# Optimization experiments

Hardware: AMD Instinct MI355X
Metric: run time of the kernel (lower is better)

Reference implementation:

```python
import jax, jax.numpy as jnp
import numpy as np

B, N, H, S, NSEC = 1, 8192, 256, 128, 8
TAU = 0.5
DEPTH_LO, DEPTH_HI = 0.0, 2.4
PADDING = 0.1
EPS = 1e-6
_p = float(np.clip(TAU, 1e-4, 1.0 - 1e-4))
LOGIT_TAU = float(np.log(_p / (1.0 - _p)))


def mlp(p, W1, b1, W2, b2, W3, b3, W4, b4):
    # p: [..., 3] -> logit [...]
    h = jax.nn.softplus(p @ W1 + b1)
    h = jax.nn.softplus(h @ W2 + b2)
    h = jax.nn.softplus(h @ W3 + b3)
    return (h @ W4 + b4)[..., 0]


def cube_intersection(ray0, rd):
    # Faithful port of check_ray_intersection_with_unit_cube.
    p_dist = 0.5 + PADDING / 2.0
    plane = jnp.concatenate([jnp.full((3,), p_dist), jnp.full((3,), -p_dist)])  # (6,)
    nom = plane - jnp.tile(ray0, (1, 1, 2))          # (B,N,6)
    den = jnp.tile(rd, (1, 1, 2))
    den = jnp.where(jnp.abs(den) < 1e-9, 1e-9, den)  # numerical guard
    d_int = nom / den                                 # (B,N,6)
    p_int = ray0[:, :, None, :] + d_int[..., None] * rd[:, :, None, :]  # (B,N,6,3)
    inside = jnp.all(jnp.abs(p_int) <= p_dist + EPS, axis=-1)           # (B,N,6)
    mask = inside.sum(-1) == 2                                           # rays hitting cube
    # pick the (exactly two) intersecting planes in ascending plane order,
    # matching torch boolean indexing semantics
    plane_id = jnp.arange(6)
    key = jnp.where(inside, plane_id, plane_id + 6)
    idx2 = jnp.argsort(key, axis=-1)[..., :2]                            # (B,N,2)
    p2 = jnp.take_along_axis(p_int, idx2[..., None], axis=2)            # (B,N,2,3)
    norm_rd = jnp.linalg.norm(rd, axis=-1)                               # (B,N)
    d2 = jnp.linalg.norm(p2 - ray0[:, :, None, :], axis=-1) / norm_rd[..., None]
    d2 = jnp.where(mask[..., None], d2, 0.0)
    d2 = jnp.sort(d2, axis=-1)
    return d2, mask


def _secant(d_low, f_low, d_high, f_high):
    den = f_high - f_low
    den = jnp.where(jnp.abs(den) < 1e-12, 1e-12, den)
    return -f_low * (d_high - d_low) / den + d_low


def reference(ray0, ray_direction, W1, b1, W2, b2, W3, b3, W4, b4):
    rd = ray_direction
    dec = lambda p: mlp(p, W1, b1, W2, b2, W3, b3, W4, b4)
    sg = jax.lax.stop_gradient

    # ---- proposal depths (no grad, as torch no_grad ray-marching) ----
    t = jnp.linspace(0.0, 1.0, S)                       # (S,)
    d_default = DEPTH_LO + t * (DEPTH_HI - DEPTH_LO)
    d2, mask_cube = cube_intersection(ray0, rd)
    d_cube = d2[..., 0:1] + t * (d2[..., 1:2] - d2[..., 0:1])   # (B,N,S)
    d_prop = jnp.where(mask_cube[..., None], d_cube, d_default)
    d_prop = sg(d_prop)

    p_prop = sg(ray0)[:, :, None, :] + d_prop[..., None] * sg(rd)[:, :, None, :]
    val = sg(dec(p_prop)) - LOGIT_TAU                   # (B,N,S)

    mask_0_not_occupied = val[..., 0] < 0
    sign_matrix = jnp.concatenate(
        [jnp.sign(val[..., :-1] * val[..., 1:]), jnp.ones(val.shape[:-1] + (1,), val.dtype)], -1)
    cost = sign_matrix * jnp.arange(S, 0, -1, dtype=val.dtype)
    idx = jnp.argmin(cost, -1)                          # first sign-change step
    vmin = jnp.min(cost, -1)
    f_low = jnp.take_along_axis(val, idx[..., None], -1)[..., 0]
    mask = (vmin < 0) & (f_low < 0) & mask_0_not_occupied

    idx_hi = jnp.minimum(idx + 1, S - 1)
    d_low = jnp.take_along_axis(d_prop, idx[..., None], -1)[..., 0]
    d_high = jnp.take_along_axis(d_prop, idx_hi[..., None], -1)[..., 0]
    f_high = jnp.take_along_axis(val, idx_hi[..., None], -1)[..., 0]

    # ---- secant refinement (no grad in torch) ----
    r0s, rds = sg(ray0), sg(rd)
    d_pred = _secant(d_low, f_low, d_high, f_high)
    for _ in range(NSEC):
        f_mid = sg(dec(r0s + d_pred[..., None] * rds)) - LOGIT_TAU
        low = f_mid < 0
        d_low = jnp.where(low, d_pred, d_low)
        f_low = jnp.where(low, f_mid, f_low)
        d_high = jnp.where(low, d_high, d_pred)
        f_high = jnp.where(low, f_high, f_mid)
        d_pred = _secant(d_low, f_low, d_high, f_high)

    # ---- differentiable implicit-gradient correction (analytic backward of
    # DepthFunction: dd/dtheta = -(df/dtheta)/(df/dd) at the surface point) ----
    d_star = sg(d_pred)
    f_of_d = lambda d: dec(ray0 + d[..., None] * rd) - LOGIT_TAU
    f_val = f_of_d(d_star)                              # differentiable wrt params/rays
    _, df_dd = jax.jvp(f_of_d, (d_star,), (jnp.ones_like(d_star),))
    df_dd = sg(df_dd)
    df_dd = jnp.where(jnp.abs(df_dd) < 1e-6,
                      jnp.where(df_dd < 0, -1e-6, 1e-6), df_dd)
    d_out = d_star - f_val / df_dd
    d_final = jnp.where(mask, d_out, 0.0)
    return d_final


def setup_inputs() -> dict:
    key = jax.random.key(0)
    ks = jax.random.split(key, 10)
    origin = jnp.array([0.0, 0.0, -1.5])
    ray0 = origin + 0.01 * jax.random.normal(ks[0], (B, N, 3), dtype=jnp.float32)
    target = jax.random.uniform(ks[1], (B, N, 3), minval=-0.4, maxval=0.4, dtype=jnp.float32)
    rd = target - ray0
    rd = rd / jnp.linalg.norm(rd, axis=-1, keepdims=True)
    W1 = jax.random.normal(ks[2], (3, H), dtype=jnp.float32) / jnp.sqrt(3.0)
    b1 = 0.1 * jax.random.normal(ks[3], (H,), dtype=jnp.float32)
    W2 = jax.random.normal(ks[4], (H, H), dtype=jnp.float32) / jnp.sqrt(float(H))
    b2 = 0.1 * jax.random.normal(ks[5], (H,), dtype=jnp.float32)
    W3 = jax.random.normal(ks[6], (H, H), dtype=jnp.float32) / jnp.sqrt(float(H))
    b3 = 0.1 * jax.random.normal(ks[7], (H,), dtype=jnp.float32)
    W4 = jax.random.normal(ks[8], (H, 1), dtype=jnp.float32) / jnp.sqrt(float(H))
    b4 = 0.1 * jax.random.normal(ks[9], (1,), dtype=jnp.float32)
    return {"ray0": ray0, "ray_direction": rd, "W1": W1, "b1": b1,
            "W2": W2, "b2": b2, "W3": W3, "b3": b3, "W4": W4, "b4": b4}
```

## Files before the change

### kernel.cpp

```cpp
#include <hip/hip_runtime.h>
#include <math.h>

#define NRAY 8192
#define SSAMP 128
#define HD 256
#define AROW 264
#define A1ROW 40
#define FIXCAP 262144
#define FIXTHR 0.018f

typedef short s16x8 __attribute__((ext_vector_type(8)));
typedef float f32x4 __attribute__((ext_vector_type(4)));

__device__ __forceinline__ unsigned short f2bf(float f) {
    unsigned u = __float_as_uint(f);
    u += 0x7fffu + ((u >> 16) & 1u);
    return (unsigned short)(u >> 16);
}
__device__ __forceinline__ float bf2f(unsigned short s) {
    return __uint_as_float(((unsigned)s) << 16);
}
__device__ __forceinline__ void split2(float f, unsigned short& hi, unsigned short& lo) {
    unsigned u = __float_as_uint(f);
    hi = (unsigned short)(u >> 16);
    float r = f - __uint_as_float(u & 0xFFFF0000u);
    lo = f2bf(r);
}
__device__ __forceinline__ unsigned pack_bf16x2(float a, float b) {
    unsigned r;
    asm("v_cvt_pk_bf16_f32 %0, %1, %2" : "=v"(r) : "v"(a), "v"(b));
    return r;
}
__device__ __forceinline__ float softplus_fast(float x) {
    return fmaxf(x, 0.0f) + __logf(1.0f + __expf(-fabsf(x)));
}
__device__ __forceinline__ float softplus_cheap(float x) {
    float m = __expf(-fabsf(x));
    float p = fmaf(m, fmaf(0.14258f, m, -0.44943f), 1.0f);
    return fmaxf(x, 0.0f) + m * p;
}
__device__ __forceinline__ float sigmoid_fast(float x) {
    return 1.0f / (1.0f + __expf(-x));
}

__global__ __launch_bounds__(256)
void prep_kernel(const float* __restrict__ W1, const float* __restrict__ b1,
                 const float* __restrict__ W2, const float* __restrict__ W3,
                 const float* __restrict__ ray0, const float* __restrict__ rdg,
                 unsigned short* __restrict__ P2, unsigned short* __restrict__ P3,
                 unsigned short* __restrict__ B1, float* __restrict__ rayinfo,
                 int* __restrict__ fix_cnt) {
    const int b = blockIdx.x, tid = threadIdx.x;
    if (b < 256) {
        int idx = b * 256 + tid;
        int k = idx >> 8, n = idx & 255;
        int nt = n >> 4, kt = k >> 5, lq = (k >> 3) & 3, j = k & 7;
        int lane = (lq << 4) | (n & 15);
        size_t off = (size_t)((nt * 8 + kt) * 2) * 512 + (size_t)lane * 8 + j;
        float w = W2[idx];
        unsigned short hi = f2bf(w);
        P2[off] = hi; P2[off + 512] = f2bf(w - bf2f(hi));
        w = W3[idx];
        hi = f2bf(w);
        P3[off] = hi; P3[off + 512] = f2bf(w - bf2f(hi));
    } else if (b < 288) {
        int idx = (b - 256) * 256 + tid;
        int w = idx & 511;
        int lane = w >> 3, j = w & 7;
        int k = ((lane >> 4) << 3) + j;
        int n = ((idx >> 9) << 4) + (lane & 15);
        unsigned short s = 0;
        if (k < 3) s = f2bf(W1[k * HD + n]);
        else if (k == 3) s = f2bf(b1[n]);
        else if (k < 7) s = f2bf(W1[(k - 4) * HD + n]);
        else if (k == 7) { unsigned short bh = f2bf(b1[n]); s = f2bf(b1[n] - bf2f(bh)); }
        else if (k < 11) { float wv = W1[(k - 8) * HD + n]; unsigned short wh = f2bf(wv); s = f2bf(wv - bf2f(wh)); }
        B1[idx] = s;
    } else {
        int r = (b - 288) * 256 + tid;
        if (r == 0) *fix_cnt = 0;
        float o0 = ray0[3 * r], o1 = ray0[3 * r + 1], o2 = ray0[3 * r + 2];
        float v0 = rdg[3 * r], v1 = rdg[3 * r + 1], v2 = rdg[3 * r + 2];
        const float pd = 0.55f, lim = pd + 1e-6f;
        float di[6]; int insk[6]; int cnt = 0;
        for (int k = 0; k < 6; k++) {
            int a = k % 3;
            float pl = (k < 3) ? pd : -pd;
            float den = (a == 0) ? v0 : ((a == 1) ? v1 : v2);
            if (fabsf(den) < 1e-9f) den = 1e-9f;
            float oa = (a == 0) ? o0 : ((a == 1) ? o1 : o2);
            float dd = (pl - oa) / den;
            float px = o0 + dd * v0, py = o1 + dd * v1, pz = o2 + dd * v2;
            int ins = (fabsf(px) <= lim) && (fabsf(py) <= lim) && (fabsf(pz) <= lim);
            di[k] = dd; insk[k] = ins; cnt += ins;
        }
        float d0 = 0.f, sl = 2.4f;
        if (cnt == 2) {
            int k1 = -1, k2 = -1;
            for (int k = 0; k < 6; k++) if (insk[k]) { if (k1 < 0) k1 = k; else k2 = k; }
            float nrd = sqrtf(v0 * v0 + v1 * v1 + v2 * v2);
            float ax = di[k1] * v0, ay = di[k1] * v1, az = di[k1] * v2;
            float d1n = sqrtf(ax * ax + ay * ay + az * az) / nrd;
            float bx = di[k2] * v0, by = di[k2] * v1, bz = di[k2] * v2;
            float d2n = sqrtf(bx * bx + by * by + bz * bz) / nrd;
            d0 = fminf(d1n, d2n);
            sl = fmaxf(d1n, d2n) - d0;
        }
        float* ri = rayinfo + (size_t)r * 8;
        ri[0] = d0; ri[1] = sl;
        ri[2] = o0; ri[3] = o1; ri[4] = o2;
        ri[5] = v0; ri[6] = v1; ri[7] = v2;
    }
}


template<int MT>
__device__ __forceinline__ void gemm_l1(const unsigned short* A1,
                                        const unsigned short* __restrict__ B1,
                                        f32x4 acc[MT][4], int lane, int ntbase) {
    const int r15 = lane & 15, q = lane >> 4;
    s16x8 wh[4];
#pragma unroll
    for (int nt = 0; nt < 4; nt++)
        wh[nt] = *(((const s16x8*)B1) + (size_t)(ntbase + nt) * 64 + lane);
#pragma unroll
    for (int mt = 0; mt < MT; mt++) {
        s16x8 ah = *(const s16x8*)(A1 + (mt * 16 + r15) * A1ROW + q * 8);
#pragma unroll
        for (int nt = 0; nt < 4; nt++)
            acc[mt][nt] = __builtin_amdgcn_mfma_f32_16x16x32_bf16(wh[nt], ah, (f32x4){0.f,0.f,0.f,0.f}, 0, 0, 0);
    }
}

template<int MT>
__device__ __forceinline__ void gemm_1t(const unsigned short* Act,
                                        const unsigned short* __restrict__ Wp,
                                        f32x4 acc[MT][4], int lane, int ntbase) {
#pragma unroll
    for (int mt = 0; mt < MT; mt++)
#pragma unroll
        for (int nt = 0; nt < 4; nt++) acc[mt][nt] = (f32x4){0.f, 0.f, 0.f, 0.f};
    const int r15 = lane & 15, q = lane >> 4;
#pragma unroll 2
    for (int kt = 0; kt < 8; kt++) {
        s16x8 wh[4];
#pragma unroll
        for (int nt = 0; nt < 4; nt++) {
            const s16x8* wp = ((const s16x8*)Wp) + (size_t)((ntbase + nt) * 8 + kt) * 128 + lane;
            wh[nt] = wp[0];
        }
        const int kc = kt * 32 + q * 8;
#pragma unroll
        for (int mt = 0; mt < MT; mt++) {
            s16x8 ah = *(const s16x8*)(Act + (mt * 16 + r15) * AROW + kc);
#pragma unroll
            for (int nt = 0; nt < 4; nt++)
                acc[mt][nt] = __builtin_amdgcn_mfma_f32_16x16x32_bf16(wh[nt], ah, acc[mt][nt], 0, 0, 0);
        }
    }
}

template<int MT>
__device__ __forceinline__ void gemm_3t(const unsigned short* Ahi, const unsigned short* Alo,
                                        const unsigned short* __restrict__ Wp,
                                        f32x4 acc[MT][4], int lane, int ntbase) {
#pragma unroll
    for (int mt = 0; mt < MT; mt++)
#pragma unroll
        for (int nt = 0; nt < 4; nt++) acc[mt][nt] = (f32x4){0.f, 0.f, 0.f, 0.f};
    const int r15 = lane & 15, q = lane >> 4;
#pragma unroll 2
    for (int kt = 0; kt < 8; kt++) {
        s16x8 wh[4], wl[4];
#pragma unroll
        for (int nt = 0; nt < 4; nt++) {
            const s16x8* wp = ((const s16x8*)Wp) + (size_t)((ntbase + nt) * 8 + kt) * 128 + lane;
            wh[nt] = wp[0];
            wl[nt] = wp[64];
        }
        const int kc = kt * 32 + q * 8;
#pragma unroll
        for (int mt = 0; mt < MT; mt++) {
            s16x8 ah = *(const s16x8*)(Ahi + (mt * 16 + r15) * AROW + kc);
            s16x8 al = *(const s16x8*)(Alo + (mt * 16 + r15) * AROW + kc);
#pragma unroll
            for (int nt = 0; nt < 4; nt++) {
                acc[mt][nt] = __builtin_amdgcn_mfma_f32_16x16x32_bf16(wh[nt], ah, acc[mt][nt], 0, 0, 0);
                acc[mt][nt] = __builtin_amdgcn_mfma_f32_16x16x32_bf16(wl[nt], ah, acc[mt][nt], 0, 0, 0);
                acc[mt][nt] = __builtin_amdgcn_mfma_f32_16x16x32_bf16(wh[nt], al, acc[mt][nt], 0, 0, 0);
            }
        }
    }
}

template<int MT>
__device__ __forceinline__ void gemm_dual(const unsigned short* Avh, const unsigned short* Avl,
                                          const unsigned short* Ath, const unsigned short* Atl,
                                          const unsigned short* __restrict__ Wp,
                                          f32x4 av[MT][4], f32x4 at[MT][4], int lane, int ntbase) {
#pragma unroll
    for (int mt = 0; mt < MT; mt++)
#pragma unroll
        for (int nt = 0; nt < 4; nt++) {
            av[mt][nt] = (f32x4){0.f, 0.f, 0.f, 0.f};
            at[mt][nt] = (f32x4){0.f, 0.f, 0.f, 0.f};
        }
    const int r15 = lane & 15, q = lane >> 4;
#pragma unroll 2
    for (int kt = 0; kt < 8; kt++) {
        s16x8 wh[4], wl[4];
#pragma unroll
        for (int nt = 0; nt < 4; nt++) {
            const s16x8* wp = ((const s16x8*)Wp) + (size_t)((ntbase + nt) * 8 + kt) * 128 + lane;
            wh[nt] = wp[0];
            wl[nt] = wp[64];
        }
        const int kc = kt * 32 + q * 8;
#pragma unroll
        for (int mt = 0; mt < MT; mt++) {
            s16x8 avhf = *(const s16x8*)(Avh + (mt * 16 + r15) * AROW + kc);
            s16x8 avlf = *(const s16x8*)(Avl + (mt * 16 + r15) * AROW + kc);
            s16x8 athf = *(const s16x8*)(Ath + (mt * 16 + r15) * AROW + kc);
            s16x8 atlf = *(const s16x8*)(Atl + (mt * 16 + r15) * AROW + kc);
#pragma unroll
            for (int nt = 0; nt < 4; nt++) {
                av[mt][nt] = __builtin_amdgcn_mfma_f32_16x16x32_bf16(wh[nt], avhf, av[mt][nt], 0, 0, 0);
                av[mt][nt] = __builtin_amdgcn_mfma_f32_16x16x32_bf16(wl[nt], avhf, av[mt][nt], 0, 0, 0);
                av[mt][nt] = __builtin_amdgcn_mfma_f32_16x16x32_bf16(wh[nt], avlf, av[mt][nt], 0, 0, 0);
                at[mt][nt] = __builtin_amdgcn_mfma_f32_16x16x32_bf16(wh[nt], athf, at[mt][nt], 0, 0, 0);
                at[mt][nt] = __builtin_amdgcn_mfma_f32_16x16x32_bf16(wl[nt], athf, at[mt][nt], 0, 0, 0);
                at[mt][nt] = __builtin_amdgcn_mfma_f32_16x16x32_bf16(wh[nt], atlf, at[mt][nt], 0, 0, 0);
            }
        }
    }
}

template<int MT>
__device__ __forceinline__ void epi_l1(f32x4 acc[MT][4], unsigned short* Ahi, int lane, int wn0) {
    const int r15 = lane & 15, q = lane >> 4;
#pragma unroll
    for (int mt = 0; mt < MT; mt++) {
        unsigned short* rowp = Ahi + (mt * 16 + r15) * AROW + wn0 + q * 4;
#pragma unroll
        for (int nt = 0; nt < 4; nt++) {
            float h0 = softplus_cheap(acc[mt][nt][0]);
            float h1 = softplus_cheap(acc[mt][nt][1]);
            float h2 = softplus_cheap(acc[mt][nt][2]);
            float h3 = softplus_cheap(acc[mt][nt][3]);
            *reinterpret_cast<uint2*>(rowp + nt * 16) =
                make_uint2(pack_bf16x2(h0, h1), pack_bf16x2(h2, h3));
        }
    }
}

template<int MT>
__device__ __forceinline__ void epi_l1_sp(f32x4 acc[MT][4], unsigned short* Ahi, unsigned short* Alo,
                                          int lane, int wn0) {
    const int r15 = lane & 15, q = lane >> 4;
#pragma unroll
    for (int mt = 0; mt < MT; mt++) {
        const int rowoff = (mt * 16 + r15) * AROW + wn0 + q * 4;
#pragma unroll
        for (int nt = 0; nt < 4; nt++) {
            float h0 = softplus_fast(acc[mt][nt][0]);
            float h1 = softplus_fast(acc[mt][nt][1]);
            float h2 = softplus_fast(acc[mt][nt][2]);
            float h3 = softplus_fast(acc[mt][nt][3]);
            unsigned x0 = pack_bf16x2(h0, h1), x1 = pack_bf16x2(h2, h3);
            float l0 = h0 - __uint_as_float(x0 << 16);
            float l1 = h1 - __uint_as_float(x0 & 0xFFFF0000u);
            float l2 = h2 - __uint_as_float(x1 << 16);
            float l3 = h3 - __uint_as_float(x1 & 0xFFFF0000u);
            *reinterpret_cast<uint2*>(Ahi + rowoff + nt * 16) = make_uint2(x0, x1);
            *reinterpret_cast<uint2*>(Alo + rowoff + nt * 16) =
                make_uint2(pack_bf16x2(l0, l1), pack_bf16x2(l2, l3));
        }
    }
}

template<int MT>
__device__ __forceinline__ void epi_hidden_1t(f32x4 acc[MT][4], const float* __restrict__ b,
                                              unsigned short* Ahi, int lane, int wn0) {
    const int r15 = lane & 15, q = lane >> 4;
    f32x4 bb[4];
#pragma unroll
    for (int nt = 0; nt < 4; nt++) bb[nt] = *(const f32x4*)(b + wn0 + nt * 16 + q * 4);
#pragma unroll
    for (int mt = 0; mt < MT; mt++) {
        unsigned short* rowp = Ahi + (mt * 16 + r15) * AROW + wn0 + q * 4;
#pragma unroll
        for (int nt = 0; nt < 4; nt++) {
            float h0 = softplus_cheap(acc[mt][nt][0] + bb[nt][0]);
            float h1 = softplus_cheap(acc[mt][nt][1] + bb[nt][1]);
            float h2 = softplus_cheap(acc[mt][nt][2] + bb[nt][2]);
            float h3 = softplus_cheap(acc[mt][nt][3] + bb[nt][3]);
            *reinterpret_cast<uint2*>(rowp + nt * 16) =
                make_uint2(pack_bf16x2(h0, h1), pack_bf16x2(h2, h3));
        }
    }
}

template<int MT>
__device__ __forceinline__ void epi_hidden_sp(f32x4 acc[MT][4], const float* __restrict__ b,
                                              unsigned short* Ahi, unsigned short* Alo,
                                              int lane, int wn0) {
    const int r15 = lane & 15, q = lane >> 4;
    f32x4 bb[4];
#pragma unroll
    for (int nt = 0; nt < 4; nt++) bb[nt] = *(const f32x4*)(b + wn0 + nt * 16 + q * 4);
#pragma unroll
    for (int mt = 0; mt < MT; mt++) {
        const int rowoff = (mt * 16 + r15) * AROW + wn0 + q * 4;
#pragma unroll
        for (int nt = 0; nt < 4; nt++) {
            float h0 = softplus_fast(acc[mt][nt][0] + bb[nt][0]);
            float h1 = softplus_fast(acc[mt][nt][1] + bb[nt][1]);
            float h2 = softplus_fast(acc[mt][nt][2] + bb[nt][2]);
            float h3 = softplus_fast(acc[mt][nt][3] + bb[nt][3]);
            unsigned x0 = pack_bf16x2(h0, h1), x1 = pack_bf16x2(h2, h3);
            float l0 = h0 - __uint_as_float(x0 << 16);
            float l1 = h1 - __uint_as_float(x0 & 0xFFFF0000u);
            float l2 = h2 - __uint_as_float(x1 << 16);
            float l3 = h3 - __uint_as_float(x1 & 0xFFFF0000u);
            *reinterpret_cast<uint2*>(Ahi + rowoff + nt * 16) = make_uint2(x0, x1);
            *reinterpret_cast<uint2*>(Alo + rowoff + nt * 16) =
                make_uint2(pack_bf16x2(l0, l1), pack_bf16x2(l2, l3));
        }
    }
}

template<int MT>
__device__ __forceinline__ void epi_dual(f32x4 av[MT][4], f32x4 at[MT][4], const float* __restrict__ b,
                                         unsigned short* Avh, unsigned short* Avl,
                                         unsigned short* Ath, unsigned short* Atl,
                                         int lane, int wn0) {
    const int r15 = lane & 15, q = lane >> 4;
    f32x4 bb[4];
#pragma unroll
    for (int nt = 0; nt < 4; nt++) bb[nt] = *(const f32x4*)(b + wn0 + nt * 16 + q * 4);
#pragma unroll
    for (int mt = 0; mt < MT; mt++) {
        const int rowoff = (mt * 16 + r15) * AROW + wn0 + q * 4;
#pragma unroll
        for (int nt = 0; nt < 4; nt++) {
            float h[4], g[4];
#pragma unroll
            for (int r = 0; r < 4; r++) {
                float z = av[mt][nt][r] + bb[nt][r];
                h[r] = softplus_fast(z);
                g[r] = sigmoid_fast(z) * at[mt][nt][r];
            }
            unsigned x0 = pack_bf16x2(h[0], h[1]), x1 = pack_bf16x2(h[2], h[3]);
            float l0 = h[0] - __uint_as_float(x0 << 16);
            float l1 = h[1] - __uint_as_float(x0 & 0xFFFF0000u);
            float l2 = h[2] - __uint_as_float(x1 << 16);
            float l3 = h[3] - __uint_as_float(x1 & 0xFFFF0000u);
            *reinterpret_cast<uint2*>(Avh + rowoff + nt * 16) = make_uint2(x0, x1);
            *reinterpret_cast<uint2*>(Avl + rowoff + nt * 16) =
                make_uint2(pack_bf16x2(l0, l1), pack_bf16x2(l2, l3));
            x0 = pack_bf16x2(g[0], g[1]); x1 = pack_bf16x2(g[2], g[3]);
            l0 = g[0] - __uint_as_float(x0 << 16);
            l1 = g[1] - __uint_as_float(x0 & 0xFFFF0000u);
            l2 = g[2] - __uint_as_float(x1 << 16);
            l3 = g[3] - __uint_as_float(x1 & 0xFFFF0000u);
            *reinterpret_cast<uint2*>(Ath + rowoff + nt * 16) = make_uint2(x0, x1);
            *reinterpret_cast<uint2*>(Atl + rowoff + nt * 16) =
                make_uint2(pack_bf16x2(l0, l1), pack_bf16x2(l2, l3));
        }
    }
}

template<int MT, bool CH>
__device__ __forceinline__ void l4_reduce(f32x4 acc[MT][4], const float* __restrict__ b3,
                                          const float* __restrict__ W4,
                                          float* partial, int lane, int wn0) {
    const int r15 = lane & 15, q = lane >> 4;
    f32x4 w4v[4], b3v[4];
#pragma unroll
    for (int nt = 0; nt < 4; nt++) {
        w4v[nt] = *(const f32x4*)(W4 + wn0 + nt * 16 + q * 4);
        b3v[nt] = *(const f32x4*)(b3 + wn0 + nt * 16 + q * 4);
    }
#pragma unroll
    for (int mt = 0; mt < MT; mt++) {
        float p = 0.f;
#pragma unroll
        for (int nt = 0; nt < 4; nt++)
#pragma unroll
            for (int r = 0; r < 4; r++) {
                float z = acc[mt][nt][r] + b3v[nt][r];
                float h = CH ? softplus_cheap(z) : softplus_fast(z);
                p = fmaf(h, w4v[nt][r], p);
            }
        p += __shfl_xor(p, 16, 64);
        p += __shfl_xor(p, 32, 64);
        if (q == 0) partial[mt * 16 + r15] = p;
    }
}

template<int MT>
__device__ __forceinline__ void l4_reduce_dual(f32x4 av[MT][4], f32x4 at[MT][4],
                                               const float* __restrict__ b3, const float* __restrict__ W4,
                                               float* pv, float* pt, int lane, int wn0) {
    const int r15 = lane & 15, q = lane >> 4;
    f32x4 w4v[4], b3v[4];
#pragma unroll
    for (int nt = 0; nt < 4; nt++) {
        w4v[nt] = *(const f32x4*)(W4 + wn0 + nt * 16 + q * 4);
        b3v[nt] = *(const f32x4*)(b3 + wn0 + nt * 16 + q * 4);
    }
#pragma unroll
    for (int mt = 0; mt < MT; mt++) {
        float sv = 0.f, st = 0.f;
#pragma unroll
        for (int nt = 0; nt < 4; nt++)
#pragma unroll
            for (int r = 0; r < 4; r++) {
                float z = av[mt][nt][r] + b3v[nt][r];
                sv = fmaf(softplus_fast(z), w4v[nt][r], sv);
                st = fmaf(sigmoid_fast(z) * at[mt][nt][r], w4v[nt][r], st);
            }
        sv += __shfl_xor(sv, 16, 64);
        sv += __shfl_xor(sv, 32, 64);
        st += __shfl_xor(st, 16, 64);
        st += __shfl_xor(st, 32, 64);
        if (q == 0) {
            pv[mt * 16 + r15] = sv;
            pt[mt * 16 + r15] = st;
        }
    }
}

__global__ __launch_bounds__(256, 4)
void coarse_mfma(const float* __restrict__ rayinfo,
                 const unsigned short* __restrict__ B1,
                 const unsigned short* __restrict__ P2, const float* __restrict__ b2,
                 const unsigned short* __restrict__ P3, const float* __restrict__ b3,
                 const float* __restrict__ W4, const float* __restrict__ b4,
                 float* __restrict__ val_out, float* __restrict__ dprop_out,
                 int* __restrict__ fix_cnt, int* __restrict__ fix_list) {
    __shared__ __align__(16) unsigned short Ahi[64 * AROW];
    __shared__ __align__(16) unsigned short A1[64 * A1ROW];
    float* partial = (float*)A1;
    const int tid = threadIdx.x;
    const int lane = tid & 63, wave = tid >> 6;
    const int r = blockIdx.x >> 1, half = blockIdx.x & 1;

    if (tid < 64) {
        const float* ri = rayinfo + (size_t)r * 8;
        const int s = half * 64 + tid;
        float t = (float)s * (1.0f / 127.0f);
        float d = fmaf(t, ri[1], ri[0]);
        dprop_out[r * SSAMP + s] = d;
        float px = fmaf(d, ri[5], ri[2]);
        float py = fmaf(d, ri[6], ri[3]);
        float pz = fmaf(d, ri[7], ri[4]);
        unsigned short hx, lx, hy, ly, hz, lz;
        split2(px, hx, lx); split2(py, hy, ly); split2(pz, hz, lz);
        unsigned short* row = A1 + tid * A1ROW;
        row[0] = hx; row[1] = hy; row[2] = hz; row[3] = 0x3F80u;
        row[4] = lx; row[5] = ly; row[6] = lz; row[7] = 0x3F80u;
        row[8] = hx; row[9] = hy; row[10] = hz;
#pragma unroll
        for (int c = 11; c < 32; c++) row[c] = 0;
    }
    __syncthreads();
    f32x4 acc[4][4];
    gemm_l1<4>(A1, B1, acc, lane, wave * 4);
    epi_l1<4>(acc, Ahi, lane, wave * 64);
    __syncthreads();
    gemm_1t<4>(Ahi, P2, acc, lane, wave * 4);
    __syncthreads();
    epi_hidden_1t<4>(acc, b2, Ahi, lane, wave * 64);
    __syncthreads();
    gemm_1t<4>(Ahi, P3, acc, lane, wave * 4);
    l4_reduce<4, true>(acc, b3, W4, &partial[wave * 64], lane, wave * 64);
    __syncthreads();
    if (tid < 64) {
        float v = partial[tid] + partial[64 + tid] + partial[128 + tid] + partial[192 + tid] + b4[0];
        int idx = r * SSAMP + half * 64 + tid;
        val_out[idx] = v;
        if (fabsf(v) < FIXTHR) {
            int pos = atomicAdd(fix_cnt, 1);
            if (pos < FIXCAP) fix_list[pos] = idx;
        }
    }
}

__global__ __launch_bounds__(256, 4)
void fixup3_mfma(const int* __restrict__ counter, const int* __restrict__ list,
                 float* __restrict__ val, const float* __restrict__ dprop,
                 const float* __restrict__ ray0, const float* __restrict__ rdg,
                 const unsigned short* __restrict__ B1,
                 const unsigned short* __restrict__ P2, const float* __restrict__ b2,
                 const unsigned short* __restrict__ P3, const float* __restrict__ b3,
                 const float* __restrict__ W4, const float* __restrict__ b4) {
    __shared__ __align__(16) unsigned short Ahi[32 * AROW];
    __shared__ __align__(16) unsigned short Alo[32 * AROW];
    __shared__ __align__(16) unsigned short A1[32 * A1ROW];
    __shared__ float partial[4][32];
    __shared__ int bidxs[32];
    const int cnt = min(*counter, FIXCAP);
    const int base = blockIdx.x * 32;
    if (base >= cnt) return;
    const int tid = threadIdx.x;
    const int lane = tid & 63, wave = tid >> 6;
    if (tid < 32) {
        const int i = min(base + tid, cnt - 1);
        const int bidx = list[i];
        bidxs[tid] = bidx;
        const int rr = bidx >> 7;
        float d = dprop[bidx];
        float px = ray0[3 * rr] + d * rdg[3 * rr];
        float py = ray0[3 * rr + 1] + d * rdg[3 * rr + 1];
        float pz = ray0[3 * rr + 2] + d * rdg[3 * rr + 2];
        unsigned short hx, lx, hy, ly, hz, lz;
        split2(px, hx, lx); split2(py, hy, ly); split2(pz, hz, lz);
        unsigned short* row = A1 + tid * A1ROW;
        row[0] = hx; row[1] = hy; row[2] = hz; row[3] = 0x3F80u;
        row[4] = lx; row[5] = ly; row[6] = lz; row[7] = 0x3F80u;
        row[8] = hx; row[9] = hy; row[10] = hz;
#pragma unroll
        for (int c = 11; c < 32; c++) row[c] = 0;
    }
    __syncthreads();
    f32x4 acc[2][4];
    gemm_l1<2>(A1, B1, acc, lane, wave * 4);
    epi_l1_sp<2>(acc, Ahi, Alo, lane, wave * 64);
    __syncthreads();
    gemm_3t<2>(Ahi, Alo, P2, acc, lane, wave * 4);
    __syncthreads();
    epi_hidden_sp<2>(acc, b2, Ahi, Alo, lane, wave * 64);
    __syncthreads();
    gemm_3t<2>(Ahi, Alo, P3, acc, lane, wave * 4);
    l4_reduce<2, false>(acc, b3, W4, &partial[wave][0], lane, wave * 64);
    __syncthreads();
    if (tid < 32) {
        float v = partial[0][tid] + partial[1][tid] + partial[2][tid] + partial[3][tid] + b4[0];
        val[bidxs[tid]] = v;
    }
}

__global__ __launch_bounds__(256, 4)
void refine_mfma(const float* __restrict__ val, const float* __restrict__ dprop,
                 const float* __restrict__ ray0, const float* __restrict__ rdg,
                 const float* __restrict__ W1, const float* __restrict__ b1,
                 const unsigned short* __restrict__ P2, const float* __restrict__ b2,
                 const unsigned short* __restrict__ P3, const float* __restrict__ b3,
                 const float* __restrict__ W4, const float* __restrict__ b4,
                 float* __restrict__ out) {
    __shared__ __align__(16) unsigned short Avh[16 * AROW];
    __shared__ __align__(16) unsigned short Avl[16 * AROW];
    __shared__ __align__(16) unsigned short Ath[16 * AROW];
    __shared__ __align__(16) unsigned short Atl[16 * AROW];
    __shared__ float partial[4][16], ptan[4][16];
    __shared__ float dl[16], fl[16], dh[16], fh[16], dps[16];
    __shared__ int mks[16];
    unsigned short* Ahi = Avh;
    const int tid = threadIdx.x;
    const int lane = tid & 63, wave = tid >> 6;
    const int r0 = blockIdx.x * 16;

    for (int i = 0; i < 4; i++) {
        const int r = r0 + wave * 4 + i;
        const float2 v = *(const float2*)(val + (size_t)r * SSAMP + lane * 2);
        const float2 dd = *(const float2*)(dprop + (size_t)r * SSAMP + lane * 2);
        float vnext = __shfl_down(v.x, 1, 64);
        const int s0 = lane * 2, s1 = s0 + 1;
        float pr0 = v.x * v.y;
        int sg0 = (pr0 > 0.f) ? 1 : ((pr0 < 0.f) ? -1 : 0);
        int k0 = (sg0 * (SSAMP - s0) + 129) * 256 + s0;
        int k1;
        if (lane == 63) {
            k1 = (1 + 129) * 256 + 127;
        } else {
            float pr1 = v.y * vnext;
            int sg1 = (pr1 > 0.f) ? 1 : ((pr1 < 0.f) ? -1 : 0);
            k1 = (sg1 * (SSAMP - s1) + 129) * 256 + s1;
        }
        int k = min(k0, k1);
#pragma unroll
        for (int m = 1; m < 64; m <<= 1) k = min(k, __shfl_xor(k, m, 64));
        int bidx = k & 255;
        int cmin = (k >> 8) - 129;
        int idxh = min(bidx + 1, SSAMP - 1);
        int ow = bidx >> 1, oh = idxh >> 1;
        float fa = __shfl(v.x, ow, 64), fb = __shfl(v.y, ow, 64);
        float da = __shfl(dd.x, ow, 64), db = __shfl(dd.y, ow, 64);
        float fa2 = __shfl(v.x, oh, 64), fb2 = __shfl(v.y, oh, 64);
        float da2 = __shfl(dd.x, oh, 64), db2 = __shfl(dd.y, oh, 64);
        float v0 = __shfl(v.x, 0, 64);
        if (lane == 0) {
            float f_low = (bidx & 1) ? fb : fa;
            float d_low = (bidx & 1) ? db : da;
            float f_high = (idxh & 1) ? fb2 : fa2;
            float d_high = (idxh & 1) ? db2 : da2;
            int sl = wave * 4 + i;
            mks[sl] = (cmin < 0) && (f_low < 0.f) && (v0 < 0.f);
            float den = f_high - f_low;
            if (fabsf(den) < 1e-12f) den = 1e-12f;
            dl[sl] = d_low; fl[sl] = f_low; dh[sl] = d_high; fh[sl] = f_high;
            dps[sl] = -f_low * (d_high - d_low) / den + d_low;
        }
    }
    __syncthreads();
    for (int it = 0; it < 8; it++) {
        {
            const int pt = tid >> 4, jb = (tid & 15) << 4;
            const int rr = r0 + pt;
            float d = dps[pt];
            float px = ray0[3 * rr] + d * rdg[3 * rr];
            float py = ray0[3 * rr + 1] + d * rdg[3 * rr + 1];
            float pz = ray0[3 * rr + 2] + d * rdg[3 * rr + 2];
            for (int j = jb; j < jb + 16; j += 4) {
                float4 wa = *(const float4*)(W1 + j);
                float4 wb = *(const float4*)(W1 + 256 + j);
                float4 wc = *(const float4*)(W1 + 512 + j);
                float4 bb = *(const float4*)(b1 + j);
                float z[4];
                z[0] = fmaf(px, wa.x, fmaf(py, wb.x, fmaf(pz, wc.x, bb.x)));
                z[1] = fmaf(px, wa.y, fmaf(py, wb.y, fmaf(pz, wc.y, bb.y)));
                z[2] = fmaf(px, wa.z, fmaf(py, wb.z, fmaf(pz, wc.z, bb.z)));
                z[3] = fmaf(px, wa.w, fmaf(py, wb.w, fmaf(pz, wc.w, bb.w)));
                *reinterpret_cast<uint2*>(&Ahi[pt * AROW + j]) =
                    make_uint2(pack_bf16x2(softplus_cheap(z[0]), softplus_cheap(z[1])),
                               pack_bf16x2(softplus_cheap(z[2]), softplus_cheap(z[3])));
            }
        }
        __syncthreads();
        f32x4 acc[1][4];
        gemm_1t<1>(Ahi, P2, acc, lane, wave * 4);
        __syncthreads();
        epi_hidden_1t<1>(acc, b2, Ahi, lane, wave * 64);
        __syncthreads();
        gemm_1t<1>(Ahi, P3, acc, lane, wave * 4);
        l4_reduce<1, true>(acc, b3, W4, &partial[wave][0], lane, wave * 64);
        __syncthreads();
        if (tid < 16) {
            float fm = partial[0][tid] + partial[1][tid] + partial[2][tid] + partial[3][tid] + b4[0];
            float dpv = dps[tid];
            float dlv = dl[tid], flv = fl[tid], dhv = dh[tid], fhv = fh[tid];
            if (fm < 0.f) { dlv = dpv; flv = fm; } else { dhv = dpv; fhv = fm; }
            float den = fhv - flv;
            if (fabsf(den) < 1e-12f) den = 1e-12f;
            dps[tid] = -flv * (dhv - dlv) / den + dlv;
            dl[tid] = dlv; fl[tid] = flv; dh[tid] = dhv; fh[tid] = fhv;
        }
        __syncthreads();
    }
    {
        const int pt = tid >> 4, jb = (tid & 15) << 4;
        const int rr = r0 + pt;
        float d = dps[pt];
        float v0 = rdg[3 * rr], v1 = rdg[3 * rr + 1], v2 = rdg[3 * rr + 2];
        float px = ray0[3 * rr] + d * v0;
        float py = ray0[3 * rr + 1] + d * v1;
        float pz = ray0[3 * rr + 2] + d * v2;
        for (int j = jb; j < jb + 16; j += 4) {
            float4 wa = *(const float4*)(W1 + j);
            float4 wb = *(const float4*)(W1 + 256 + j);
            float4 wc = *(const float4*)(W1 + 512 + j);
            float4 bb = *(const float4*)(b1 + j);
            float z[4], zt[4], h[4], g[4];
            z[0] = fmaf(px, wa.x, fmaf(py, wb.x, fmaf(pz, wc.x, bb.x)));
            z[1] = fmaf(px, wa.y, fmaf(py, wb.y, fmaf(pz, wc.y, bb.y)));
            z[2] = fmaf(px, wa.z, fmaf(py, wb.z, fmaf(pz, wc.z, bb.z)));
            z[3] = fmaf(px, wa.w, fmaf(py, wb.w, fmaf(pz, wc.w, bb.w)));
            zt[0] = fmaf(v0, wa.x, fmaf(v1, wb.x, v2 * wc.x));
            zt[1] = fmaf(v0, wa.y, fmaf(v1, wb.y, v2 * wc.y));
            zt[2] = fmaf(v0, wa.z, fmaf(v1, wb.z, v2 * wc.z));
            zt[3] = fmaf(v0, wa.w, fmaf(v1, wb.w, v2 * wc.w));
#pragma unroll
            for (int i = 0; i < 4; i++) {
                h[i] = softplus_fast(z[i]);
                g[i] = sigmoid_fast(z[i]) * zt[i];
            }
            unsigned x0 = pack_bf16x2(h[0], h[1]), x1 = pack_bf16x2(h[2], h[3]);
            float l0 = h[0] - __uint_as_float(x0 << 16);
            float l1 = h[1] - __uint_as_float(x0 & 0xFFFF0000u);
            float l2 = h[2] - __uint_as_float(x1 << 16);
            float l3 = h[3] - __uint_as_float(x1 & 0xFFFF0000u);
            *reinterpret_cast<uint2*>(&Avh[pt * AROW + j]) = make_uint2(x0, x1);
            *reinterpret_cast<uint2*>(&Avl[pt * AROW + j]) =
                make_uint2(pack_bf16x2(l0, l1), pack_bf16x2(l2, l3));
            x0 = pack_bf16x2(g[0], g[1]); x1 = pack_bf16x2(g[2], g[3]);
            l0 = g[0] - __uint_as_float(x0 << 16);
            l1 = g[1] - __uint_as_float(x0 & 0xFFFF0000u);
            l2 = g[2] - __uint_as_float(x1 << 16);
            l3 = g[3] - __uint_as_float(x1 & 0xFFFF0000u);
            *reinterpret_cast<uint2*>(&Ath[pt * AROW + j]) = make_uint2(x0, x1);
            *reinterpret_cast<uint2*>(&Atl[pt * AROW + j]) =
                make_uint2(pack_bf16x2(l0, l1), pack_bf16x2(l2, l3));
        }
    }
    __syncthreads();
    f32x4 av[1][4], at[1][4];
    gemm_dual<1>(Avh, Avl, Ath, Atl, P2, av, at, lane, wave * 4);
    __syncthreads();
    epi_dual<1>(av, at, b2, Avh, Avl, Ath, Atl, lane, wave * 64);
    __syncthreads();
    gemm_dual<1>(Avh, Avl, Ath, Atl, P3, av, at, lane, wave * 4);
    l4_reduce_dual<1>(av, at, b3, W4, &partial[wave][0], &ptan[wave][0], lane, wave * 64);
    __syncthreads();
    if (tid < 16) {
        float f = partial[0][tid] + partial[1][tid] + partial[2][tid] + partial[3][tid] + b4[0];
        float ft = ptan[0][tid] + ptan[1][tid] + ptan[2][tid] + ptan[3][tid];
        if (fabsf(ft) < 1e-6f) ft = (ft < 0.f) ? -1e-6f : 1e-6f;
        float dres = dps[tid] - f / ft;
        out[r0 + tid] = mks[tid] ? dres : 0.0f;
    }
}

extern "C" void kernel_launch(void* const* d_in, const int* in_sizes, int n_in,
                              void* d_out, int out_size, void* d_ws, size_t ws_size,
                              hipStream_t stream) {
    const float* ray0 = (const float*)d_in[0];
    const float* rdg  = (const float*)d_in[1];
    const float* W1 = (const float*)d_in[2];
    const float* b1 = (const float*)d_in[3];
    const float* W2 = (const float*)d_in[4];
    const float* b2 = (const float*)d_in[5];
    const float* W3 = (const float*)d_in[6];
    const float* b3 = (const float*)d_in[7];
    const float* W4 = (const float*)d_in[8];
    const float* b4 = (const float*)d_in[9];
    float* out = (float*)d_out;

    float* ws = (float*)d_ws;
    float* val    = ws;
    float* dprop  = ws + (size_t)SSAMP * NRAY;
    unsigned short* P2 = (unsigned short*)(ws + (size_t)2 * SSAMP * NRAY);
    unsigned short* P3 = P2 + 131072;
    unsigned short* B1 = P3 + 131072;
    float* rayinfo = (float*)(B1 + 8192);
    int* fix_cnt  = (int*)(rayinfo + (size_t)NRAY * 8);
    int* fix_list = fix_cnt + 64;

    hipLaunchKernelGGL(prep_kernel, dim3(320), dim3(256), 0, stream,
                       W1, b1, W2, W3, ray0, rdg, P2, P3, B1, rayinfo, fix_cnt);
    hipLaunchKernelGGL(coarse_mfma, dim3(NRAY * 2), dim3(256), 0, stream,
                       rayinfo, B1, P2, b2, P3, b3, W4, b4, val, dprop, fix_cnt, fix_list);
    hipLaunchKernelGGL(fixup3_mfma, dim3(FIXCAP / 32), dim3(256), 0, stream,
                       fix_cnt, fix_list, val, dprop, ray0, rdg,
                       B1, P2, b2, P3, b3, W4, b4);
    hipLaunchKernelGGL(refine_mfma, dim3(NRAY / 16), dim3(256), 0, stream,
                       val, dprop, ray0, rdg, W1, b1, P2, b2, P3, b3, W4, b4, out);
}
```

Before: 708.5 us.

## Split coarse MLP work across eight waves with narrower per-wave column tiles

Templates the MFMA GEMM and epilogue helpers on the number of N-tiles per wave. The coarse kernel moves to 512 threads (8 waves), with each wave covering 32 output columns instead of 64, and the final partial-sum reduction loops over 8 waves. This cuts per-wave accumulator registers and adds waves per block, aiming for more latency hiding. In exchange, weight-fragment reuse per activation load drops and the larger block means more barrier cost; the launch bound now requests 6 blocks of 512 threads per CU. The other kernels keep NT=4, so their behaviour is unchanged.

```diff
diff --git a/kernel.cpp b/kernel.cpp
--- a/kernel.cpp
+++ b/kernel.cpp
@@ -114,38 +114,38 @@
 }
 
 
-template<int MT>
+template<int MT, int NT>
 __device__ __forceinline__ void gemm_l1(const unsigned short* A1,
                                         const unsigned short* __restrict__ B1,
-                                        f32x4 acc[MT][4], int lane, int ntbase) {
-    const int r15 = lane & 15, q = lane >> 4;
-    s16x8 wh[4];
-#pragma unroll
-    for (int nt = 0; nt < 4; nt++)
+                                        f32x4 acc[MT][NT], int lane, int ntbase) {
+    const int r15 = lane & 15, q = lane >> 4;
+    s16x8 wh[NT];
+#pragma unroll
+    for (int nt = 0; nt < NT; nt++)
         wh[nt] = *(((const s16x8*)B1) + (size_t)(ntbase + nt) * 64 + lane);
 #pragma unroll
     for (int mt = 0; mt < MT; mt++) {
         s16x8 ah = *(const s16x8*)(A1 + (mt * 16 + r15) * A1ROW + q * 8);
 #pragma unroll
-        for (int nt = 0; nt < 4; nt++)
+        for (int nt = 0; nt < NT; nt++)
             acc[mt][nt] = __builtin_amdgcn_mfma_f32_16x16x32_bf16(wh[nt], ah, (f32x4){0.f,0.f,0.f,0.f}, 0, 0, 0);
     }
 }
 
-template<int MT>
+template<int MT, int NT>
 __device__ __forceinline__ void gemm_1t(const unsigned short* Act,
                                         const unsigned short* __restrict__ Wp,
-                                        f32x4 acc[MT][4], int lane, int ntbase) {
+                                        f32x4 acc[MT][NT], int lane, int ntbase) {
 #pragma unroll
     for (int mt = 0; mt < MT; mt++)
 #pragma unroll
-        for (int nt = 0; nt < 4; nt++) acc[mt][nt] = (f32x4){0.f, 0.f, 0.f, 0.f};
+        for (int nt = 0; nt < NT; nt++) acc[mt][nt] = (f32x4){0.f, 0.f, 0.f, 0.f};
     const int r15 = lane & 15, q = lane >> 4;
 #pragma unroll 2
     for (int kt = 0; kt < 8; kt++) {
-        s16x8 wh[4];
-#pragma unroll
-        for (int nt = 0; nt < 4; nt++) {
+        s16x8 wh[NT];
+#pragma unroll
+        for (int nt = 0; nt < NT; nt++) {
             const s16x8* wp = ((const s16x8*)Wp) + (size_t)((ntbase + nt) * 8 + kt) * 128 + lane;
             wh[nt] = wp[0];
         }
@@ -154,26 +154,26 @@
         for (int mt = 0; mt < MT; mt++) {
             s16x8 ah = *(const s16x8*)(Act + (mt * 16 + r15) * AROW + kc);
 #pragma unroll
-            for (int nt = 0; nt < 4; nt++)
+            for (int nt = 0; nt < NT; nt++)
                 acc[mt][nt] = __builtin_amdgcn_mfma_f32_16x16x32_bf16(wh[nt], ah, acc[mt][nt], 0, 0, 0);
         }
     }
 }
 
-template<int MT>
+template<int MT, int NT>
 __device__ __forceinline__ void gemm_3t(const unsigned short* Ahi, const unsigned short* Alo,
                                         const unsigned short* __restrict__ Wp,
-                                        f32x4 acc[MT][4], int lane, int ntbase) {
+                                        f32x4 acc[MT][NT], int lane, int ntbase) {
 #pragma unroll
     for (int mt = 0; mt < MT; mt++)
 #pragma unroll
-        for (int nt = 0; nt < 4; nt++) acc[mt][nt] = (f32x4){0.f, 0.f, 0.f, 0.f};
+        for (int nt = 0; nt < NT; nt++) acc[mt][nt] = (f32x4){0.f, 0.f, 0.f, 0.f};
     const int r15 = lane & 15, q = lane >> 4;
 #pragma unroll 2
     for (int kt = 0; kt < 8; kt++) {
-        s16x8 wh[4], wl[4];
-#pragma unroll
-        for (int nt = 0; nt < 4; nt++) {
+        s16x8 wh[NT], wl[NT];
+#pragma unroll
+        for (int nt = 0; nt < NT; nt++) {
             const s16x8* wp = ((const s16x8*)Wp) + (size_t)((ntbase + nt) * 8 + kt) * 128 + lane;
             wh[nt] = wp[0];
             wl[nt] = wp[64];
@@ -184,7 +184,7 @@
             s16x8 ah = *(const s16x8*)(Ahi + (mt * 16 + r15) * AROW + kc);
             s16x8 al = *(const s16x8*)(Alo + (mt * 16 + r15) * AROW + kc);
 #pragma unroll
-            for (int nt = 0; nt < 4; nt++) {
+            for (int nt = 0; nt < NT; nt++) {
                 acc[mt][nt] = __builtin_amdgcn_mfma_f32_16x16x32_bf16(wh[nt], ah, acc[mt][nt], 0, 0, 0);
                 acc[mt][nt] = __builtin_amdgcn_mfma_f32_16x16x32_bf16(wl[nt], ah, acc[mt][nt], 0, 0, 0);
                 acc[mt][nt] = __builtin_amdgcn_mfma_f32_16x16x32_bf16(wh[nt], al, acc[mt][nt], 0, 0, 0);
@@ -193,24 +193,24 @@
     }
 }
 
-template<int MT>
+template<int MT, int NT>
 __device__ __forceinline__ void gemm_dual(const unsigned short* Avh, const unsigned short* Avl,
                                           const unsigned short* Ath, const unsigned short* Atl,
                                           const unsigned short* __restrict__ Wp,
-                                          f32x4 av[MT][4], f32x4 at[MT][4], int lane, int ntbase) {
+                                          f32x4 av[MT][NT], f32x4 at[MT][NT], int lane, int ntbase) {
 #pragma unroll
     for (int mt = 0; mt < MT; mt++)
 #pragma unroll
-        for (int nt = 0; nt < 4; nt++) {
+        for (int nt = 0; nt < NT; nt++) {
             av[mt][nt] = (f32x4){0.f, 0.f, 0.f, 0.f};
             at[mt][nt] = (f32x4){0.f, 0.f, 0.f, 0.f};
         }
     const int r15 = lane & 15, q = lane >> 4;
 #pragma unroll 2
     for (int kt = 0; kt < 8; kt++) {
-        s16x8 wh[4], wl[4];
-#pragma unroll
-        for (int nt = 0; nt < 4; nt++) {
+        s16x8 wh[NT], wl[NT];
+#pragma unroll
+        for (int nt = 0; nt < NT; nt++) {
             const s16x8* wp = ((const s16x8*)Wp) + (size_t)((ntbase + nt) * 8 + kt) * 128 + lane;
             wh[nt] = wp[0];
             wl[nt] = wp[64];
@@ -223,7 +223,7 @@
             s16x8 athf = *(const s16x8*)(Ath + (mt * 16 + r15) * AROW + kc);
             s16x8 atlf = *(const s16x8*)(Atl + (mt * 16 + r15) * AROW + kc);
 #pragma unroll
-            for (int nt = 0; nt < 4; nt++) {
+            for (int nt = 0; nt < NT; nt++) {
                 av[mt][nt] = __builtin_amdgcn_mfma_f32_16x16x32_bf16(wh[nt], avhf, av[mt][nt], 0, 0, 0);
                 av[mt][nt] = __builtin_amdgcn_mfma_f32_16x16x32_bf16(wl[nt], avhf, av[mt][nt], 0, 0, 0);
                 av[mt][nt] = __builtin_amdgcn_mfma_f32_16x16x32_bf16(wh[nt], avlf, av[mt][nt], 0, 0, 0);
@@ -235,14 +235,14 @@
     }
 }
 
-template<int MT>
-__device__ __forceinline__ void epi_l1(f32x4 acc[MT][4], unsigned short* Ahi, int lane, int wn0) {
+template<int MT, int NT>
+__device__ __forceinline__ void epi_l1(f32x4 acc[MT][NT], unsigned short* Ahi, int lane, int wn0) {
     const int r15 = lane & 15, q = lane >> 4;
 #pragma unroll
     for (int mt = 0; mt < MT; mt++) {
         unsigned short* rowp = Ahi + (mt * 16 + r15) * AROW + wn0 + q * 4;
 #pragma unroll
-        for (int nt = 0; nt < 4; nt++) {
+        for (int nt = 0; nt < NT; nt++) {
             float h0 = softplus_cheap(acc[mt][nt][0]);
             float h1 = softplus_cheap(acc[mt][nt][1]);
             float h2 = softplus_cheap(acc[mt][nt][2]);
@@ -253,15 +253,15 @@
     }
 }
 
-template<int MT>
-__device__ __forceinline__ void epi_l1_sp(f32x4 acc[MT][4], unsigned short* Ahi, unsigned short* Alo,
+template<int MT, int NT>
+__device__ __forceinline__ void epi_l1_sp(f32x4 acc[MT][NT], unsigned short* Ahi, unsigned short* Alo,
                                           int lane, int wn0) {
     const int r15 = lane & 15, q = lane >> 4;
 #pragma unroll
     for (int mt = 0; mt < MT; mt++) {
         const int rowoff = (mt * 16 + r15) * AROW + wn0 + q * 4;
 #pragma unroll
-        for (int nt = 0; nt < 4; nt++) {
+        for (int nt = 0; nt < NT; nt++) {
             float h0 = softplus_fast(acc[mt][nt][0]);
             float h1 = softplus_fast(acc[mt][nt][1]);
             float h2 = softplus_fast(acc[mt][nt][2]);
@@ -278,18 +278,18 @@
     }
 }
 
-template<int MT>
-__device__ __forceinline__ void epi_hidden_1t(f32x4 acc[MT][4], const float* __restrict__ b,
+template<int MT, int NT>
+__device__ __forceinline__ void epi_hidden_1t(f32x4 acc[MT][NT], const float* __restrict__ b,
                                               unsigned short* Ahi, int lane, int wn0) {
     const int r15 = lane & 15, q = lane >> 4;
-    f32x4 bb[4];
-#pragma unroll
-    for (int nt = 0; nt < 4; nt++) bb[nt] = *(const f32x4*)(b + wn0 + nt * 16 + q * 4);
+    f32x4 bb[NT];
+#pragma unroll
+    for (int nt = 0; nt < NT; nt++) bb[nt] = *(const f32x4*)(b + wn0 + nt * 16 + q * 4);
 #pragma unroll
     for (int mt = 0; mt < MT; mt++) {
         unsigned short* rowp = Ahi + (mt * 16 + r15) * AROW + wn0 + q * 4;
 #pragma unroll
-        for (int nt = 0; nt < 4; nt++) {
+        for (int nt = 0; nt < NT; nt++) {
             float h0 = softplus_cheap(acc[mt][nt][0] + bb[nt][0]);
             float h1 = softplus_cheap(acc[mt][nt][1] + bb[nt][1]);
             float h2 = softplus_cheap(acc[mt][nt][2] + bb[nt][2]);
@@ -300,19 +300,19 @@
     }
 }
 
-template<int MT>
-__device__ __forceinline__ void epi_hidden_sp(f32x4 acc[MT][4], const float* __restrict__ b,
+template<int MT, int NT>
+__device__ __forceinline__ void epi_hidden_sp(f32x4 acc[MT][NT], const float* __restrict__ b,
                                               unsigned short* Ahi, unsigned short* Alo,
                                               int lane, int wn0) {
     const int r15 = lane & 15, q = lane >> 4;
-    f32x4 bb[4];
-#pragma unroll
-    for (int nt = 0; nt < 4; nt++) bb[nt] = *(const f32x4*)(b + wn0 + nt * 16 + q * 4);
+    f32x4 bb[NT];
+#pragma unroll
+    for (int nt = 0; nt < NT; nt++) bb[nt] = *(const f32x4*)(b + wn0 + nt * 16 + q * 4);
 #pragma unroll
     for (int mt = 0; mt < MT; mt++) {
         const int rowoff = (mt * 16 + r15) * AROW + wn0 + q * 4;
 #pragma unroll
-        for (int nt = 0; nt < 4; nt++) {
+        for (int nt = 0; nt < NT; nt++) {
             float h0 = softplus_fast(acc[mt][nt][0] + bb[nt][0]);
             float h1 = softplus_fast(acc[mt][nt][1] + bb[nt][1]);
             float h2 = softplus_fast(acc[mt][nt][2] + bb[nt][2]);
@@ -329,20 +329,20 @@
     }
 }
 
-template<int MT>
-__device__ __forceinline__ void epi_dual(f32x4 av[MT][4], f32x4 at[MT][4], const float* __restrict__ b,
+template<int MT, int NT>
+__device__ __forceinline__ void epi_dual(f32x4 av[MT][NT], f32x4 at[MT][NT], const float* __restrict__ b,
                                          unsigned short* Avh, unsigned short* Avl,
                                          unsigned short* Ath, unsigned short* Atl,
                                          int lane, int wn0) {
     const int r15 = lane & 15, q = lane >> 4;
-    f32x4 bb[4];
-#pragma unroll
-    for (int nt = 0; nt < 4; nt++) bb[nt] = *(const f32x4*)(b + wn0 + nt * 16 + q * 4);
+    f32x4 bb[NT];
+#pragma unroll
+    for (int nt = 0; nt < NT; nt++) bb[nt] = *(const f32x4*)(b + wn0 + nt * 16 + q * 4);
 #pragma unroll
     for (int mt = 0; mt < MT; mt++) {
         const int rowoff = (mt * 16 + r15) * AROW + wn0 + q * 4;
 #pragma unroll
-        for (int nt = 0; nt < 4; nt++) {
+        for (int nt = 0; nt < NT; nt++) {
             float h[4], g[4];
 #pragma unroll
             for (int r = 0; r < 4; r++) {
@@ -370,14 +370,14 @@
     }
 }
 
-template<int MT, bool CH>
-__device__ __forceinline__ void l4_reduce(f32x4 acc[MT][4], const float* __restrict__ b3,
+template<int MT, int NT, bool CH>
+__device__ __forceinline__ void l4_reduce(f32x4 acc[MT][NT], const float* __restrict__ b3,
                                           const float* __restrict__ W4,
                                           float* partial, int lane, int wn0) {
     const int r15 = lane & 15, q = lane >> 4;
-    f32x4 w4v[4], b3v[4];
-#pragma unroll
-    for (int nt = 0; nt < 4; nt++) {
+    f32x4 w4v[NT], b3v[NT];
+#pragma unroll
+    for (int nt = 0; nt < NT; nt++) {
         w4v[nt] = *(const f32x4*)(W4 + wn0 + nt * 16 + q * 4);
         b3v[nt] = *(const f32x4*)(b3 + wn0 + nt * 16 + q * 4);
     }
@@ -385,7 +385,7 @@
     for (int mt = 0; mt < MT; mt++) {
         float p = 0.f;
 #pragma unroll
-        for (int nt = 0; nt < 4; nt++)
+        for (int nt = 0; nt < NT; nt++)
 #pragma unroll
             for (int r = 0; r < 4; r++) {
                 float z = acc[mt][nt][r] + b3v[nt][r];
@@ -398,14 +398,14 @@
     }
 }
 
-template<int MT>
-__device__ __forceinline__ void l4_reduce_dual(f32x4 av[MT][4], f32x4 at[MT][4],
+template<int MT, int NT>
+__device__ __forceinline__ void l4_reduce_dual(f32x4 av[MT][NT], f32x4 at[MT][NT],
                                                const float* __restrict__ b3, const float* __restrict__ W4,
                                                float* pv, float* pt, int lane, int wn0) {
     const int r15 = lane & 15, q = lane >> 4;
-    f32x4 w4v[4], b3v[4];
-#pragma unroll
-    for (int nt = 0; nt < 4; nt++) {
+    f32x4 w4v[NT], b3v[NT];
+#pragma unroll
+    for (int nt = 0; nt < NT; nt++) {
         w4v[nt] = *(const f32x4*)(W4 + wn0 + nt * 16 + q * 4);
         b3v[nt] = *(const f32x4*)(b3 + wn0 + nt * 16 + q * 4);
     }
@@ -413,7 +413,7 @@
     for (int mt = 0; mt < MT; mt++) {
         float sv = 0.f, st = 0.f;
 #pragma unroll
-        for (int nt = 0; nt < 4; nt++)
+        for (int nt = 0; nt < NT; nt++)
 #pragma unroll
             for (int r = 0; r < 4; r++) {
                 float z = av[mt][nt][r] + b3v[nt][r];
@@ -431,7 +431,7 @@
     }
 }
 
-__global__ __launch_bounds__(256, 4)
+__global__ __launch_bounds__(512, 6)
 void coarse_mfma(const float* __restrict__ rayinfo,
                  const unsigned short* __restrict__ B1,
                  const unsigned short* __restrict__ P2, const float* __restrict__ b2,
@@ -465,19 +465,21 @@
         for (int c = 11; c < 32; c++) row[c] = 0;
     }
     __syncthreads();
-    f32x4 acc[4][4];
-    gemm_l1<4>(A1, B1, acc, lane, wave * 4);
-    epi_l1<4>(acc, Ahi, lane, wave * 64);
-    __syncthreads();
-    gemm_1t<4>(Ahi, P2, acc, lane, wave * 4);
-    __syncthreads();
-    epi_hidden_1t<4>(acc, b2, Ahi, lane, wave * 64);
-    __syncthreads();
-    gemm_1t<4>(Ahi, P3, acc, lane, wave * 4);
-    l4_reduce<4, true>(acc, b3, W4, &partial[wave * 64], lane, wave * 64);
+    f32x4 acc[4][2];
+    gemm_l1<4, 2>(A1, B1, acc, lane, wave * 2);
+    epi_l1<4, 2>(acc, Ahi, lane, wave * 32);
+    __syncthreads();
+    gemm_1t<4, 2>(Ahi, P2, acc, lane, wave * 2);
+    __syncthreads();
+    epi_hidden_1t<4, 2>(acc, b2, Ahi, lane, wave * 32);
+    __syncthreads();
+    gemm_1t<4, 2>(Ahi, P3, acc, lane, wave * 2);
+    l4_reduce<4, 2, true>(acc, b3, W4, &partial[wave * 64], lane, wave * 32);
     __syncthreads();
     if (tid < 64) {
-        float v = partial[tid] + partial[64 + tid] + partial[128 + tid] + partial[192 + tid] + b4[0];
+        float v = b4[0];
+#pragma unroll
+        for (int w = 0; w < 8; w++) v += partial[w * 64 + tid];
         int idx = r * SSAMP + half * 64 + tid;
         val_out[idx] = v;
         if (fabsf(v) < FIXTHR) {
@@ -525,15 +527,15 @@
     }
     __syncthreads();
     f32x4 acc[2][4];
-    gemm_l1<2>(A1, B1, acc, lane, wave * 4);
-    epi_l1_sp<2>(acc, Ahi, Alo, lane, wave * 64);
-    __syncthreads();
-    gemm_3t<2>(Ahi, Alo, P2, acc, lane, wave * 4);
-    __syncthreads();
-    epi_hidden_sp<2>(acc, b2, Ahi, Alo, lane, wave * 64);
-    __syncthreads();
-    gemm_3t<2>(Ahi, Alo, P3, acc, lane, wave * 4);
-    l4_reduce<2, false>(acc, b3, W4, &partial[wave][0], lane, wave * 64);
+    gemm_l1<2, 4>(A1, B1, acc, lane, wave * 4);
+    epi_l1_sp<2, 4>(acc, Ahi, Alo, lane, wave * 64);
+    __syncthreads();
+    gemm_3t<2, 4>(Ahi, Alo, P2, acc, lane, wave * 4);
+    __syncthreads();
+    epi_hidden_sp<2, 4>(acc, b2, Ahi, Alo, lane, wave * 64);
+    __syncthreads();
+    gemm_3t<2, 4>(Ahi, Alo, P3, acc, lane, wave * 4);
+    l4_reduce<2, 4, false>(acc, b3, W4, &partial[wave][0], lane, wave * 64);
     __syncthreads();
     if (tid < 32) {
         float v = partial[0][tid] + partial[1][tid] + partial[2][tid] + partial[3][tid] + b4[0];
@@ -629,12 +631,12 @@
         }
         __syncthreads();
         f32x4 acc[1][4];
-        gemm_1t<1>(Ahi, P2, acc, lane, wave * 4);
+        gemm_1t<1, 4>(Ahi, P2, acc, lane, wave * 4);
         __syncthreads();
-        epi_hidden_1t<1>(acc, b2, Ahi, lane, wave * 64);
+        epi_hidden_1t<1, 4>(acc, b2, Ahi, lane, wave * 64);
         __syncthreads();
-        gemm_1t<1>(Ahi, P3, acc, lane, wave * 4);
-        l4_reduce<1, true>(acc, b3, W4, &partial[wave][0], lane, wave * 64);
+        gemm_1t<1, 4>(Ahi, P3, acc, lane, wave * 4);
+        l4_reduce<1, 4, true>(acc, b3, W4, &partial[wave][0], lane, wave * 64);
         __syncthreads();
         if (tid < 16) {
             float fm = partial[0][tid] + partial[1][tid] + partial[2][tid] + partial[3][tid] + b4[0];
@@ -695,12 +697,12 @@
     }
     __syncthreads();
     f32x4 av[1][4], at[1][4];
-    gemm_dual<1>(Avh, Avl, Ath, Atl, P2, av, at, lane, wave * 4);
-    __syncthreads();
-    epi_dual<1>(av, at, b2, Avh, Avl, Ath, Atl, lane, wave * 64);
-    __syncthreads();
-    gemm_dual<1>(Avh, Avl, Ath, Atl, P3, av, at, lane, wave * 4);
-    l4_reduce_dual<1>(av, at, b3, W4, &partial[wave][0], &ptan[wave][0], lane, wave * 64);
+    gemm_dual<1, 4>(Avh, Avl, Ath, Atl, P2, av, at, lane, wave * 4);
+    __syncthreads();
+    epi_dual<1, 4>(av, at, b2, Avh, Avl, Ath, Atl, lane, wave * 64);
+    __syncthreads();
+    gemm_dual<1, 4>(Avh, Avl, Ath, Atl, P3, av, at, lane, wave * 4);
+    l4_reduce_dual<1, 4>(av, at, b3, W4, &partial[wave][0], &ptan[wave][0], lane, wave * 64);
     __syncthreads();
     if (tid < 16) {
         float f = partial[0][tid] + partial[1][tid] + partial[2][tid] + partial[3][tid] + b4[0];
@@ -738,7 +740,7 @@
 
     hipLaunchKernelGGL(prep_kernel, dim3(320), dim3(256), 0, stream,
                        W1, b1, W2, W3, ray0, rdg, P2, P3, B1, rayinfo, fix_cnt);
-    hipLaunchKernelGGL(coarse_mfma, dim3(NRAY * 2), dim3(256), 0, stream,
+    hipLaunchKernelGGL(coarse_mfma, dim3(NRAY * 2), dim3(512), 0, stream,
                        rayinfo, B1, P2, b2, P3, b3, W4, b4, val, dprop, fix_cnt, fix_list);
     hipLaunchKernelGGL(fixup3_mfma, dim3(FIXCAP / 32), dim3(256), 0, stream,
                        fix_cnt, fix_list, val, dprop, ray0, rdg,
```

Result: slower. 725.6 us (+2.4%).
